# Kernel optimization log

Measured on AMD Instinct MI355X. Metric: run time of the kernel, lower is better.

The kernel has to match this reference:

```python
import jax, jax.numpy as jnp
import numpy as np

NEG_SLOPE = 0.1  # LReLu_neg_slope
WEIGHT_INIT_STD = 1.0
N_GEN, N_LOAD, N_END = 25000, 25000, 25000
N_NODES = 100000
N_EDGES = 1600000
H = 128
N_HIDDEN_LAYERS = 3  # N_GCN_layers - 1


def _lin_w(key, n_in, n_out):
    # torch init: normal(std = weight_init_std / in_channels); stored as (in, out) for jax
    return jax.random.normal(key, (n_in, n_out), dtype=jnp.float32) * (WEIGHT_INIT_STD / n_in)


def setup_inputs() -> dict:
    key = jax.random.key(0)
    ks = jax.random.split(key, 24)
    inp = {
        "x_gen": jax.random.normal(ks[0], (N_GEN, 3), dtype=jnp.float32),
        "x_load": jax.random.normal(ks[1], (N_LOAD, 3), dtype=jnp.float32),
        "x_or": jax.random.normal(ks[2], (N_END, 6), dtype=jnp.float32),
        "x_ex": jax.random.normal(ks[3], (N_END, 6), dtype=jnp.float32),
        "edge_index": jax.random.randint(ks[4], (2, N_EDGES), 0, N_NODES, dtype=jnp.int64)
        if jax.config.jax_enable_x64 else jax.random.randint(ks[4], (2, N_EDGES), 0, N_NODES, dtype=jnp.int32),
        "object_ptv": jnp.arange(N_NODES, dtype=jnp.int32),
    }
    # per-type embedding MLPs (2 Linear layers each)
    inp["Wg1"], inp["bg1"] = _lin_w(ks[5], 3, H), jnp.zeros((H,), jnp.float32)
    inp["Wg2"], inp["bg2"] = _lin_w(ks[6], H, H), jnp.zeros((H,), jnp.float32)
    inp["Wld1"], inp["bld1"] = _lin_w(ks[7], 3, H), jnp.zeros((H,), jnp.float32)
    inp["Wld2"], inp["bld2"] = _lin_w(ks[8], H, H), jnp.zeros((H,), jnp.float32)
    inp["Wor1"], inp["bor1"] = _lin_w(ks[9], 6, H), jnp.zeros((H,), jnp.float32)
    inp["Wor2"], inp["bor2"] = _lin_w(ks[10], H, H), jnp.zeros((H,), jnp.float32)
    inp["Wex1"], inp["bex1"] = _lin_w(ks[11], 6, H), jnp.zeros((H,), jnp.float32)
    inp["Wex2"], inp["bex2"] = _lin_w(ks[12], H, H), jnp.zeros((H,), jnp.float32)
    # hidden SAGEConv layers (stacked): lin_l (neighbor, with bias) + lin_r (root, no bias)
    inp["Wl_h"] = jnp.stack([_lin_w(ks[13 + i], H, H) for i in range(N_HIDDEN_LAYERS)])
    inp["bl_h"] = jnp.zeros((N_HIDDEN_LAYERS, H), jnp.float32)
    inp["Wr_h"] = jnp.stack([_lin_w(ks[16 + i], H, H) for i in range(N_HIDDEN_LAYERS)])
    # output SAGEConv layer -> 1 unit
    inp["Wl_o"], inp["bl_o"] = _lin_w(ks[19], H, 1), jnp.zeros((1,), jnp.float32)
    inp["Wr_o"] = _lin_w(ks[20], H, 1)
    return inp


def _lrelu(x):
    return jax.nn.leaky_relu(x, NEG_SLOPE)


def _embed(x, W1, b1, W2, b2):
    return _lrelu(_lrelu(x @ W1 + b1) @ W2 + b2)


def reference(x_gen, x_load, x_or, x_ex, edge_index, object_ptv,
              Wg1, bg1, Wg2, bg2, Wld1, bld1, Wld2, bld2,
              Wor1, bor1, Wor2, bor2, Wex1, bex1, Wex2, bex2,
              Wl_h, bl_h, Wr_h, Wl_o, bl_o, Wr_o):
    x = jnp.concatenate([
        _embed(x_gen, Wg1, bg1, Wg2, bg2),
        _embed(x_load, Wld1, bld1, Wld2, bld2),
        _embed(x_or, Wor1, bor1, Wor2, bor2),
        _embed(x_ex, Wex1, bex1, Wex2, bex2),
    ], axis=0)
    x = x[object_ptv]                      # [N, H] in topology-vector order
    src, dst = edge_index[0], edge_index[1]
    n = x.shape[0]
    deg = jax.ops.segment_sum(jnp.ones_like(src, dtype=x.dtype), dst, num_segments=n)
    inv_deg = (1.0 / jnp.maximum(deg, 1.0))[:, None]

    def sage(h, Wl, bl, Wr):
        # SAGEConv(aggr='mean', root_weight=True): lin_l(mean_j h_j) + bias + lin_r(h_i)
        agg = jax.ops.segment_sum(h[src], dst, num_segments=n) * inv_deg
        return agg @ Wl + bl + h @ Wr

    for i in range(Wl_h.shape[0]):
        x = _lrelu(sage(x, Wl_h[i], bl_h[i], Wr_h[i]))
    return jax.nn.sigmoid(sage(x, Wl_o, bl_o, Wr_o))  # [N, 1]
```

## Files before the change

### kernel.cpp

```cpp
#include <hip/hip_runtime.h>
#include <hip/hip_bf16.h>
#include <math.h>

#define HD 128
#define NPB 512
#define CAP 16384
#define SCHUNK 4096
#define ALCSR 768

typedef __attribute__((ext_vector_type(8))) short  bf16x8;
typedef __attribute__((ext_vector_type(4))) float  f32x4;

__device__ __forceinline__ float lrelu(float v) { return v > 0.0f ? v : 0.1f * v; }

__device__ __forceinline__ unsigned short f2bf(float f) {
  union { float f; unsigned u; } c; c.f = f;
  unsigned u = c.u + 0x7fffu + ((c.u >> 16) & 1u);
  return (unsigned short)(u >> 16);
}
__device__ __forceinline__ float bf2f(unsigned short u) {
  return __uint_as_float((unsigned)u << 16);
}

__global__ __launch_bounds__(256)
void embed1_kernel(const float* __restrict__ xg, const float* __restrict__ xl,
                   const float* __restrict__ xo, const float* __restrict__ xe,
                   const float* __restrict__ Wg, const float* __restrict__ bg,
                   const float* __restrict__ Wl, const float* __restrict__ bl,
                   const float* __restrict__ Wo, const float* __restrict__ bo,
                   const float* __restrict__ We, const float* __restrict__ be,
                   unsigned short* __restrict__ h1, int4 padCum, int4 realCnt) {
  int p = blockIdx.x * 2 + (threadIdx.x >> 7);
  if (p >= padCum.w) return;
  int j = threadIdx.x & 127;
  int typ = (p < padCum.x) ? 0 : (p < padCum.y) ? 1 : (p < padCum.z) ? 2 : 3;
  int padStart = (typ == 0) ? 0 : (typ == 1) ? padCum.x : (typ == 2) ? padCum.y : padCum.z;
  int cnt = (typ == 0) ? realCnt.x : (typ == 1) ? realCnt.y : (typ == 2) ? realCnt.z : realCnt.w;
  int loc = p - padStart;
  if (loc >= cnt) return;
  const float *x, *W, *bb; int IN;
  if (typ == 0)      { x = xg; W = Wg; bb = bg; IN = 3; }
  else if (typ == 1) { x = xl; W = Wl; bb = bl; IN = 3; }
  else if (typ == 2) { x = xo; W = Wo; bb = bo; IN = 6; }
  else               { x = xe; W = We; bb = be; IN = 6; }
  float acc = bb[j];
  for (int k = 0; k < IN; k++) acc += x[(size_t)loc * IN + k] * W[k * HD + j];
  h1[(size_t)p * HD + j] = f2bf(lrelu(acc));
}

__global__ __launch_bounds__(256)
void wprep_all_kernel(const float* __restrict__ Wg2, const float* __restrict__ Wld2,
                      const float* __restrict__ Wor2, const float* __restrict__ Wex2,
                      const float* __restrict__ Wl_h, const float* __restrict__ Wr_h,
                      unsigned short* __restrict__ Wp,
                      const int* __restrict__ ptv, int* __restrict__ inv,
                      int* __restrict__ gcnt, int n) {
  int tid = blockIdx.x * 256 + threadIdx.x;
  if (tid < 256) gcnt[tid] = 0;
  if (tid < n) inv[ptv[tid]] = tid;
  int m = tid >> 14;
  int i = tid & 16383;
  const float* src; unsigned short* dst;
  switch (m) {
    case 0: src = Wg2;  dst = Wp;             break;
    case 1: src = Wld2; dst = Wp + 16384;     break;
    case 2: src = Wor2; dst = Wp + 2 * 16384; break;
    case 3: src = Wex2; dst = Wp + 3 * 16384; break;
    default: {
      int mm = m - 4; int l = mm >> 1; int isR = mm & 1;
      src = (isR ? Wr_h : Wl_h) + (size_t)l * 16384;
      dst = Wp + 4 * 16384 + (size_t)l * 32768 + (isR ? 16384 : 0);
    }
  }
  int k = i >> 7, j = i & 127;
  int ks = k >> 5, g = (k >> 3) & 3, b = k & 7;
  dst[((ks * 128 + j) * 4 + g) * 8 + b] = f2bf(src[i]);
}

__global__ __launch_bounds__(256)
void mfma_embed2_kernel(const unsigned short* __restrict__ h1,
                        const unsigned short* __restrict__ Wp,
                        const float* __restrict__ b_g, const float* __restrict__ b_ld,
                        const float* __restrict__ b_or, const float* __restrict__ b_ex,
                        const int* __restrict__ inv, unsigned short* __restrict__ out,
                        int4 padCum, int4 realStart, int4 realCnt) {
  const int t = threadIdx.x, w = t >> 6, l = t & 63;
  const int lr = l & 15, lg = l >> 4;
  const int prow0 = blockIdx.x * 64 + w * 16;
  int typ = (prow0 < padCum.x) ? 0 : (prow0 < padCum.y) ? 1 : (prow0 < padCum.z) ? 2 : 3;
  int padStart = (typ == 0) ? 0 : (typ == 1) ? padCum.x : (typ == 2) ? padCum.y : padCum.z;
  int rStart = (typ == 0) ? realStart.x : (typ == 1) ? realStart.y : (typ == 2) ? realStart.z : realStart.w;
  int cnt = (typ == 0) ? realCnt.x : (typ == 1) ? realCnt.y : (typ == 2) ? realCnt.z : realCnt.w;
  const float* bias = (typ == 0) ? b_g : (typ == 1) ? b_ld : (typ == 2) ? b_or : b_ex;

  int raLoc = prow0 + lr - padStart; if (raLoc >= cnt) raLoc = cnt - 1;
  const unsigned short* abase = h1 + (size_t)(padStart + raLoc) * HD + 8 * lg;
  const unsigned short* wbase = Wp + (size_t)typ * 16384 + lr * 32 + lg * 8;

  f32x4 acc[8];
  #pragma unroll
  for (int cb = 0; cb < 8; cb++) {
    float bv = bias[cb * 16 + lr];
    acc[cb] = (f32x4){bv, bv, bv, bv};
  }
  #pragma unroll
  for (int ks = 0; ks < 4; ks++) {
    bf16x8 af = *(const bf16x8*)(abase + ks * 32);
    #pragma unroll
    for (int cb = 0; cb < 8; cb++) {
      bf16x8 bfv = *(const bf16x8*)(wbase + (size_t)(ks * 128 + cb * 16) * 32);
      acc[cb] = __builtin_amdgcn_mfma_f32_16x16x32_bf16(af, bfv, acc[cb], 0, 0, 0);
    }
  }
  int tgt[4];
  #pragma unroll
  for (int r = 0; r < 4; r++) {
    int locRow = prow0 + lg * 4 + r - padStart;
    tgt[r] = (locRow < cnt) ? inv[rStart + locRow] : -1;
  }
  #pragma unroll
  for (int cb = 0; cb < 8; cb++) {
    #pragma unroll
    for (int r = 0; r < 4; r++) {
      if (tgt[r] >= 0)
        out[(size_t)tgt[r] * HD + cb * 16 + lr] = f2bf(lrelu(acc[cb][r]));
    }
  }
}

__global__ __launch_bounds__(256)
void bucket_scatter_kernel(const int* __restrict__ esrc, const int* __restrict__ edst,
                           int* __restrict__ gcnt, int* __restrict__ ebuf, int nE) {
  __shared__ int cnt[256];
  __shared__ int cur[256];
  const int t = threadIdx.x;
  const int c0 = blockIdx.x * SCHUNK;
  int s_arr[16], d_arr[16];
  cnt[t] = 0;
  __syncthreads();
  #pragma unroll
  for (int k = 0; k < 16; k++) {
    int idx = c0 + k * 256 + t;
    if (idx < nE) {
      s_arr[k] = esrc[idx];
      int d = edst[idx];
      d_arr[k] = d;
      atomicAdd(&cnt[d >> 9], 1);
    } else d_arr[k] = -1;
  }
  __syncthreads();
  if (cnt[t] > 0) cur[t] = atomicAdd(&gcnt[t], cnt[t]);
  __syncthreads();
  #pragma unroll
  for (int k = 0; k < 16; k++) {
    if (d_arr[k] >= 0) {
      int b = d_arr[k] >> 9;
      int p = atomicAdd(&cur[b], 1);
      ebuf[(size_t)b * CAP + p] = (s_arr[k] << 9) | (d_arr[k] & 511);
    }
  }
}

__device__ __forceinline__ int wave_incl_scan(int v) {
  int lane = threadIdx.x & 63;
  #pragma unroll
  for (int d = 1; d < 64; d <<= 1) {
    int tv = __shfl_up(v, d, 64);
    if (lane >= d) v += tv;
  }
  return v;
}

__global__ __launch_bounds__(256)
void bucket_build_kernel(const int* __restrict__ ebuf, const int* __restrict__ gcnt,
                         int* __restrict__ csr, int* __restrict__ offs,
                         int* __restrict__ deg, float* __restrict__ inv_deg, int n) {
  __shared__ int hist[512];
  __shared__ int offl[512];
  __shared__ int wsum[4];
  const int b = blockIdx.x, t = threadIdx.x;
  const int cnt = gcnt[b];
  const size_t ebase = (size_t)b * CAP;
  hist[t] = 0; hist[t + 256] = 0;
  __syncthreads();
  for (int i = t; i < cnt; i += 256) {
    int e = ebuf[ebase + i];
    atomicAdd(&hist[e & 511], 1);
  }
  __syncthreads();
  int a0 = hist[2 * t], a1 = hist[2 * t + 1];
  int s = a0 + a1;
  int incl = wave_incl_scan(s);
  int wid = t >> 6;
  if ((t & 63) == 63) wsum[wid] = incl;
  __syncthreads();
  int wbase = 0;
  for (int w_ = 0; w_ < wid; w_++) wbase += wsum[w_];
  int excl = wbase + incl - s;
  offl[2 * t] = excl;
  offl[2 * t + 1] = excl + a0;
  __syncthreads();
  const int d0 = b << 9;
  for (int i = t; i < 512; i += 256) {
    int g = d0 + i;
    if (g < n) {
      offs[g] = b * CAP + offl[i];
      int dg = hist[i];
      deg[g] = dg;
      inv_deg[g] = 1.0f / fmaxf((float)dg, 1.0f);
    }
  }
  __syncthreads();
  for (int i = t; i < cnt; i += 256) {
    int e = ebuf[ebase + i];
    int p = atomicAdd(&offl[e & 511], 1);
    csr[ebase + p] = ((unsigned)e) >> 9;
  }
}

template<bool EMIT_Z>
__global__ __launch_bounds__(256)
void sage_fused_kernel(const unsigned short* __restrict__ x, const int* __restrict__ csr,
                       const int* __restrict__ offs, const int* __restrict__ deg,
                       const float* __restrict__ inv_deg,
                       const unsigned short* __restrict__ Wp, const float* __restrict__ bias,
                       unsigned short* __restrict__ out,
                       const float* __restrict__ wl, const float* __restrict__ wr,
                       float* __restrict__ zl, float* __restrict__ zr, int n) {
  __shared__ int lcsr[ALCSR];
  __shared__ __align__(16) unsigned short lagg[16][136];
  __shared__ float zpart[2][4][16];
  const int t = threadIdx.x;
  const int node0 = blockIdx.x * 16;
  int last = node0 + 15; if (last >= n) last = n - 1;
  const int s_begin = offs[node0];
  const int total = offs[last] + deg[last] - s_begin;
  const bool useLds = (total <= ALCSR);
  if (useLds) {
    for (int k = t; k < total; k += 256) lcsr[k] = csr[s_begin + k];
  }
  __syncthreads();

  const int w = t >> 6, l = t & 63;
  {
    const int g = l >> 4, j = l & 15;
    const int node = node0 + w * 4 + g;
    if (node < n) {
      const unsigned short* xj = x + 8 * j;
      const int lb = offs[node] - s_begin;
      const int d = deg[node];
      float2 a0[4] = {{0.f,0.f},{0.f,0.f},{0.f,0.f},{0.f,0.f}};
      float2 a1[4] = {{0.f,0.f},{0.f,0.f},{0.f,0.f},{0.f,0.f}};
      auto acc4 = [](float2* A, uint4 v) {
        A[0].x += __uint_as_float(v.x << 16); A[0].y += __uint_as_float(v.x & 0xffff0000u);
        A[1].x += __uint_as_float(v.y << 16); A[1].y += __uint_as_float(v.y & 0xffff0000u);
        A[2].x += __uint_as_float(v.z << 16); A[2].y += __uint_as_float(v.z & 0xffff0000u);
        A[3].x += __uint_as_float(v.w << 16); A[3].y += __uint_as_float(v.w & 0xffff0000u);
      };
      int i = 0;
      if (useLds) {
        for (; i + 3 < d; i += 4) {
          int e0 = lcsr[lb + i], e1 = lcsr[lb + i + 1];
          int e2 = lcsr[lb + i + 2], e3 = lcsr[lb + i + 3];
          uint4 v0 = *(const uint4*)(xj + (size_t)e0 * HD);
          uint4 v1 = *(const uint4*)(xj + (size_t)e1 * HD);
          uint4 v2 = *(const uint4*)(xj + (size_t)e2 * HD);
          uint4 v3 = *(const uint4*)(xj + (size_t)e3 * HD);
          acc4(a0, v0); acc4(a1, v1); acc4(a0, v2); acc4(a1, v3);
        }
        if (i + 1 < d) {
          int e0 = lcsr[lb + i], e1 = lcsr[lb + i + 1];
          uint4 v0 = *(const uint4*)(xj + (size_t)e0 * HD);
          uint4 v1 = *(const uint4*)(xj + (size_t)e1 * HD);
          acc4(a0, v0); acc4(a1, v1);
          i += 2;
        }
        if (i < d) {
          int e0 = lcsr[lb + i];
          acc4(a0, *(const uint4*)(xj + (size_t)e0 * HD));
        }
      } else {
        const int* gcsr = csr + s_begin + lb;
        for (; i + 3 < d; i += 4) {
          int e0 = gcsr[i], e1 = gcsr[i + 1], e2 = gcsr[i + 2], e3 = gcsr[i + 3];
          uint4 v0 = *(const uint4*)(xj + (size_t)e0 * HD);
          uint4 v1 = *(const uint4*)(xj + (size_t)e1 * HD);
          uint4 v2 = *(const uint4*)(xj + (size_t)e2 * HD);
          uint4 v3 = *(const uint4*)(xj + (size_t)e3 * HD);
          acc4(a0, v0); acc4(a1, v1); acc4(a0, v2); acc4(a1, v3);
        }
        if (i + 1 < d) {
          int e0 = gcsr[i], e1 = gcsr[i + 1];
          uint4 v0 = *(const uint4*)(xj + (size_t)e0 * HD);
          uint4 v1 = *(const uint4*)(xj + (size_t)e1 * HD);
          acc4(a0, v0); acc4(a1, v1);
          i += 2;
        }
        if (i < d) {
          int e0 = gcsr[i];
          acc4(a0, *(const uint4*)(xj + (size_t)e0 * HD));
        }
      }
      const float id = inv_deg[node];
      uint4 o;
      unsigned* op = (unsigned*)&o;
      #pragma unroll
      for (int k = 0; k < 4; k++) {
        float lo = (a0[k].x + a1[k].x) * id;
        float hi = (a0[k].y + a1[k].y) * id;
        op[k] = (unsigned)f2bf(lo) | ((unsigned)f2bf(hi) << 16);
      }
      *(uint4*)&lagg[w * 4 + g][j * 8] = o;
    } else {
      *(uint4*)&lagg[w * 4 + g][j * 8] = make_uint4(0, 0, 0, 0);
    }
  }
  __syncthreads();

  const int lr = l & 15, lg = l >> 4;
  int ra = node0 + lr; if (ra >= n) ra = n - 1;
  const unsigned short* wbase = Wp + (size_t)lr * 32 + (size_t)lg * 8;
  const unsigned short* rbase = x + (size_t)ra * HD + 8 * lg;

  f32x4 acc[2];
  #pragma unroll
  for (int c = 0; c < 2; c++) {
    float bv = bias[(2 * w + c) * 16 + lr];
    acc[c] = (f32x4){bv, bv, bv, bv};
  }
  #pragma unroll
  for (int ks = 0; ks < 4; ks++) {
    bf16x8 af = *(const bf16x8*)&lagg[lr][lg * 8 + ks * 32];
    #pragma unroll
    for (int c = 0; c < 2; c++) {
      int cb = 2 * w + c;
      bf16x8 bfv = *(const bf16x8*)(wbase + (size_t)(ks * 128 + cb * 16) * 32);
      acc[c] = __builtin_amdgcn_mfma_f32_16x16x32_bf16(af, bfv, acc[c], 0, 0, 0);
    }
  }
  #pragma unroll
  for (int ks = 0; ks < 4; ks++) {
    bf16x8 af = *(const bf16x8*)(rbase + ks * 32);
    #pragma unroll
    for (int c = 0; c < 2; c++) {
      int cb = 2 * w + c;
      bf16x8 bfv = *(const bf16x8*)(wbase + (size_t)((4 + ks) * 128 + cb * 16) * 32);
      acc[c] = __builtin_amdgcn_mfma_f32_16x16x32_bf16(af, bfv, acc[c], 0, 0, 0);
    }
  }

  if constexpr (!EMIT_Z) {
    #pragma unroll
    for (int c = 0; c < 2; c++) {
      int cb = 2 * w + c;
      #pragma unroll
      for (int r = 0; r < 4; r++) {
        int node = node0 + lg * 4 + r;
        if (node < n)
          out[(size_t)node * HD + cb * 16 + lr] = f2bf(lrelu(acc[c][r]));
      }
    }
  } else {
    float vl[4] = {0.f, 0.f, 0.f, 0.f}, vr[4] = {0.f, 0.f, 0.f, 0.f};
    #pragma unroll
    for (int c = 0; c < 2; c++) {
      int cb = 2 * w + c;
      float wlv = wl[cb * 16 + lr];
      float wrv = wr[cb * 16 + lr];
      #pragma unroll
      for (int r = 0; r < 4; r++) {
        float x3 = lrelu(acc[c][r]);
        vl[r] += x3 * wlv;
        vr[r] += x3 * wrv;
      }
    }
    #pragma unroll
    for (int r = 0; r < 4; r++) {
      #pragma unroll
      for (int d = 1; d < 16; d <<= 1) {
        vl[r] += __shfl_xor(vl[r], d, 64);
        vr[r] += __shfl_xor(vr[r], d, 64);
      }
    }
    if (lr == 0) {
      #pragma unroll
      for (int r = 0; r < 4; r++) {
        zpart[0][w][lg * 4 + r] = vl[r];
        zpart[1][w][lg * 4 + r] = vr[r];
      }
    }
    __syncthreads();
    if (t < 16) {
      int node = node0 + t;
      if (node < n) {
        zl[node] = zpart[0][0][t] + zpart[0][1][t] + zpart[0][2][t] + zpart[0][3][t];
        zr[node] = zpart[1][0][t] + zpart[1][1][t] + zpart[1][2][t] + zpart[1][3][t];
      }
    }
  }
}

__global__ __launch_bounds__(256)
void zfinal_kernel(const float* __restrict__ zl, const float* __restrict__ zr,
                   const int* __restrict__ csr, const int* __restrict__ offs,
                   const int* __restrict__ deg, const float* __restrict__ inv_deg,
                   const float* __restrict__ bl, float* __restrict__ out, int n) {
  int i = blockIdx.x * 256 + threadIdx.x;
  if (i >= n) return;
  int s0 = offs[i], d = deg[i];
  float a = 0.f;
  #pragma unroll 4
  for (int e = 0; e < d; e++) a += zl[csr[s0 + e]];
  float s = a * inv_deg[i] + bl[0] + zr[i];
  out[i] = 1.0f / (1.0f + expf(-s));
}

extern "C" void kernel_launch(void* const* d_in, const int* in_sizes, int n_in,
                              void* d_out, int out_size, void* d_ws, size_t ws_size,
                              hipStream_t stream) {
  const float* x_gen  = (const float*)d_in[0];
  const float* x_load = (const float*)d_in[1];
  const float* x_or   = (const float*)d_in[2];
  const float* x_ex   = (const float*)d_in[3];
  const int*   edge   = (const int*)d_in[4];
  const int*   ptv    = (const int*)d_in[5];
  const float* Wg1  = (const float*)d_in[6],  *bg1  = (const float*)d_in[7];
  const float* Wg2  = (const float*)d_in[8],  *bg2  = (const float*)d_in[9];
  const float* Wld1 = (const float*)d_in[10], *bld1 = (const float*)d_in[11];
  const float* Wld2 = (const float*)d_in[12], *bld2 = (const float*)d_in[13];
  const float* Wor1 = (const float*)d_in[14], *bor1 = (const float*)d_in[15];
  const float* Wor2 = (const float*)d_in[16], *bor2 = (const float*)d_in[17];
  const float* Wex1 = (const float*)d_in[18], *bex1 = (const float*)d_in[19];
  const float* Wex2 = (const float*)d_in[20], *bex2 = (const float*)d_in[21];
  const float* Wl_h = (const float*)d_in[22], *bl_h = (const float*)d_in[23];
  const float* Wr_h = (const float*)d_in[24];
  const float* Wl_o = (const float*)d_in[25], *bl_o = (const float*)d_in[26];
  const float* Wr_o = (const float*)d_in[27];

  const int n_gen  = in_sizes[0] / 3;
  const int n_load = in_sizes[1] / 3;
  const int n_or   = in_sizes[2] / 6;
  const int n_ex   = in_sizes[3] / 6;
  const int nE     = in_sizes[4] / 2;
  const int N      = in_sizes[5];
  const int* esrc = edge;
  const int* edst = edge + nE;

  const int np0 = ((n_gen  + 63) / 64) * 64;
  const int np1 = ((n_load + 63) / 64) * 64;
  const int np2 = ((n_or   + 63) / 64) * 64;
  const int np3 = ((n_ex   + 63) / 64) * 64;
  const int NP  = np0 + np1 + np2 + np3;
  const int4 padCum    = make_int4(np0, np0 + np1, np0 + np1 + np2, NP);
  const int4 realStart = make_int4(0, n_gen, n_gen + n_load, n_gen + n_load + n_or);
  const int4 realCnt   = make_int4(n_gen, n_load, n_or, n_ex);

  const int NB = (N + NPB - 1) / NPB;

  size_t NPel = (size_t)NP * HD;
  size_t nel  = (size_t)N * HD;
  unsigned short* b0 = (unsigned short*)d_ws;
  unsigned short* b1 = b0 + NPel;
  unsigned short* b3 = b1 + nel;
  int*  gcnt = (int*)(b3 + nel);
  int*  ebuf = gcnt + 256;
  int*  csr  = ebuf + (size_t)NB * CAP;
  int*  offs = csr + (size_t)NB * CAP;
  int*  deg  = offs + N;
  float* inv_deg = (float*)(deg + N);
  float* zl = inv_deg + N;
  float* zr = zl + N;
  int*  invp = (int*)(zr + N);
  uintptr_t wp_addr = ((uintptr_t)(invp + N) + 15) & ~(uintptr_t)15;
  unsigned short* Wp = (unsigned short*)wp_addr;

  wprep_all_kernel<<<640, 256, 0, stream>>>(Wg2, Wld2, Wor2, Wex2, Wl_h, Wr_h, Wp,
                                            ptv, invp, gcnt, N);

  embed1_kernel<<<NP / 2, 256, 0, stream>>>(x_gen, x_load, x_or, x_ex,
                                            Wg1, bg1, Wld1, bld1, Wor1, bor1, Wex1, bex1,
                                            b0, padCum, realCnt);
  mfma_embed2_kernel<<<NP / 64, 256, 0, stream>>>(b0, Wp, bg2, bld2, bor2, bex2,
                                                  invp, b1, padCum, realStart, realCnt);

  bucket_scatter_kernel<<<(nE + SCHUNK - 1) / SCHUNK, 256, 0, stream>>>(esrc, edst, gcnt, ebuf, nE);
  bucket_build_kernel<<<NB, 256, 0, stream>>>(ebuf, gcnt, csr, offs, deg, inv_deg, N);

  const int fGrid = (N + 15) / 16;
  const unsigned short* WpC = Wp + 4 * 16384;
  unsigned short* xcur = b1;
  unsigned short* xnext = b3;
  for (int l = 0; l < 2; l++) {
    sage_fused_kernel<false><<<fGrid, 256, 0, stream>>>(
        xcur, csr, offs, deg, inv_deg, WpC + (size_t)l * 32768,
        bl_h + (size_t)l * HD, xnext, nullptr, nullptr, nullptr, nullptr, N);
    unsigned short* tmp = xcur; xcur = xnext; xnext = tmp;
  }
  sage_fused_kernel<true><<<fGrid, 256, 0, stream>>>(
      xcur, csr, offs, deg, inv_deg, WpC + 2 * 32768,
      bl_h + 2 * HD, nullptr, Wl_o, Wr_o, zl, zr, N);

  zfinal_kernel<<<(N + 255) / 256, 256, 0, stream>>>(zl, zr, csr, offs, deg, inv_deg,
                                                     bl_o, (float*)d_out, N);
}
```

Before: 347.0 us.

## Gather neighbor features in FP8 E5M2 to halve aggregation bandwidth

Keeps a second copy of node features in FP8 E5M2, produced by a new conversion kernel after the embedding and written alongside the bf16 output of each hidden SAGE layer. The neighbor-mean gather then reads 8 bytes per lane instead of 16, aiming to cut memory traffic in the bandwidth-bound aggregation. The cost is an extra conversion pass, extra byte stores, and a large loss of precision in the aggregated features that may break accuracy tolerance. The root term still uses the bf16 copy.

```diff
diff --git a/kernel.cpp b/kernel.cpp
--- a/kernel.cpp
+++ b/kernel.cpp
@@ -1,5 +1,6 @@
 #include <hip/hip_runtime.h>
 #include <hip/hip_bf16.h>
+#include <hip/hip_fp16.h>
 #include <math.h>
 
 #define HD 128
@@ -20,6 +21,14 @@
 }
 __device__ __forceinline__ float bf2f(unsigned short u) {
   return __uint_as_float((unsigned)u << 16);
+}
+__device__ __forceinline__ unsigned char f2e5m2(float f) {
+  unsigned short h = __half_as_ushort(__float2half(f));
+  h = (unsigned short)(h + 0x7f + ((h >> 8) & 1));
+  return (unsigned char)(h >> 8);
+}
+__device__ __forceinline__ float e5m2hi2f(unsigned u) {
+  return __half2float(__ushort_as_half((unsigned short)u));
 }
 
 __global__ __launch_bounds__(256)
@@ -129,6 +138,25 @@
 }
 
 __global__ __launch_bounds__(256)
+void bf2f8_kernel(const unsigned short* __restrict__ in, unsigned char* __restrict__ out, int n8) {
+  int idx = blockIdx.x * 256 + threadIdx.x;
+  if (idx >= n8) return;
+  uint4 v = *(const uint4*)(in + (size_t)idx * 8);
+  unsigned char b0 = f2e5m2(__uint_as_float(v.x << 16));
+  unsigned char b1 = f2e5m2(__uint_as_float(v.x & 0xffff0000u));
+  unsigned char b2 = f2e5m2(__uint_as_float(v.y << 16));
+  unsigned char b3 = f2e5m2(__uint_as_float(v.y & 0xffff0000u));
+  unsigned char b4 = f2e5m2(__uint_as_float(v.z << 16));
+  unsigned char b5 = f2e5m2(__uint_as_float(v.z & 0xffff0000u));
+  unsigned char b6 = f2e5m2(__uint_as_float(v.w << 16));
+  unsigned char b7 = f2e5m2(__uint_as_float(v.w & 0xffff0000u));
+  uint2 o;
+  o.x = (unsigned)b0 | ((unsigned)b1 << 8) | ((unsigned)b2 << 16) | ((unsigned)b3 << 24);
+  o.y = (unsigned)b4 | ((unsigned)b5 << 8) | ((unsigned)b6 << 16) | ((unsigned)b7 << 24);
+  *(uint2*)(out + (size_t)idx * 8) = o;
+}
+
+__global__ __launch_bounds__(256)
 void bucket_scatter_kernel(const int* __restrict__ esrc, const int* __restrict__ edst,
                            int* __restrict__ gcnt, int* __restrict__ ebuf, int nE) {
   __shared__ int cnt[256];
@@ -220,11 +248,12 @@
 
 template<bool EMIT_Z>
 __global__ __launch_bounds__(256)
-void sage_fused_kernel(const unsigned short* __restrict__ x, const int* __restrict__ csr,
+void sage_fused_kernel(const unsigned short* __restrict__ x, const unsigned char* __restrict__ xf8,
+                       const int* __restrict__ csr,
                        const int* __restrict__ offs, const int* __restrict__ deg,
                        const float* __restrict__ inv_deg,
                        const unsigned short* __restrict__ Wp, const float* __restrict__ bias,
-                       unsigned short* __restrict__ out,
+                       unsigned short* __restrict__ out, unsigned char* __restrict__ outf8,
                        const float* __restrict__ wl, const float* __restrict__ wr,
                        float* __restrict__ zl, float* __restrict__ zr, int n) {
   __shared__ int lcsr[ALCSR];
@@ -246,59 +275,63 @@
     const int g = l >> 4, j = l & 15;
     const int node = node0 + w * 4 + g;
     if (node < n) {
-      const unsigned short* xj = x + 8 * j;
+      const unsigned char* xj = xf8 + 8 * j;
       const int lb = offs[node] - s_begin;
       const int d = deg[node];
       float2 a0[4] = {{0.f,0.f},{0.f,0.f},{0.f,0.f},{0.f,0.f}};
       float2 a1[4] = {{0.f,0.f},{0.f,0.f},{0.f,0.f},{0.f,0.f}};
-      auto acc4 = [](float2* A, uint4 v) {
-        A[0].x += __uint_as_float(v.x << 16); A[0].y += __uint_as_float(v.x & 0xffff0000u);
-        A[1].x += __uint_as_float(v.y << 16); A[1].y += __uint_as_float(v.y & 0xffff0000u);
-        A[2].x += __uint_as_float(v.z << 16); A[2].y += __uint_as_float(v.z & 0xffff0000u);
-        A[3].x += __uint_as_float(v.w << 16); A[3].y += __uint_as_float(v.w & 0xffff0000u);
+      auto acc8 = [](float2* A, uint2 v) {
+        A[0].x += e5m2hi2f((v.x << 8) & 0xff00u);
+        A[0].y += e5m2hi2f(v.x & 0xff00u);
+        A[1].x += e5m2hi2f((v.x >> 8) & 0xff00u);
+        A[1].y += e5m2hi2f((v.x >> 16) & 0xff00u);
+        A[2].x += e5m2hi2f((v.y << 8) & 0xff00u);
+        A[2].y += e5m2hi2f(v.y & 0xff00u);
+        A[3].x += e5m2hi2f((v.y >> 8) & 0xff00u);
+        A[3].y += e5m2hi2f((v.y >> 16) & 0xff00u);
       };
       int i = 0;
       if (useLds) {
         for (; i + 3 < d; i += 4) {
           int e0 = lcsr[lb + i], e1 = lcsr[lb + i + 1];
           int e2 = lcsr[lb + i + 2], e3 = lcsr[lb + i + 3];
-          uint4 v0 = *(const uint4*)(xj + (size_t)e0 * HD);
-          uint4 v1 = *(const uint4*)(xj + (size_t)e1 * HD);
-          uint4 v2 = *(const uint4*)(xj + (size_t)e2 * HD);
-          uint4 v3 = *(const uint4*)(xj + (size_t)e3 * HD);
-          acc4(a0, v0); acc4(a1, v1); acc4(a0, v2); acc4(a1, v3);
+          uint2 v0 = *(const uint2*)(xj + (size_t)e0 * HD);
+          uint2 v1 = *(const uint2*)(xj + (size_t)e1 * HD);
+          uint2 v2 = *(const uint2*)(xj + (size_t)e2 * HD);
+          uint2 v3 = *(const uint2*)(xj + (size_t)e3 * HD);
+          acc8(a0, v0); acc8(a1, v1); acc8(a0, v2); acc8(a1, v3);
         }
         if (i + 1 < d) {
           int e0 = lcsr[lb + i], e1 = lcsr[lb + i + 1];
-          uint4 v0 = *(const uint4*)(xj + (size_t)e0 * HD);
-          uint4 v1 = *(const uint4*)(xj + (size_t)e1 * HD);
-          acc4(a0, v0); acc4(a1, v1);
+          uint2 v0 = *(const uint2*)(xj + (size_t)e0 * HD);
+          uint2 v1 = *(const uint2*)(xj + (size_t)e1 * HD);
+          acc8(a0, v0); acc8(a1, v1);
           i += 2;
         }
         if (i < d) {
           int e0 = lcsr[lb + i];
-          acc4(a0, *(const uint4*)(xj + (size_t)e0 * HD));
+          acc8(a0, *(const uint2*)(xj + (size_t)e0 * HD));
         }
       } else {
         const int* gcsr = csr + s_begin + lb;
         for (; i + 3 < d; i += 4) {
           int e0 = gcsr[i], e1 = gcsr[i + 1], e2 = gcsr[i + 2], e3 = gcsr[i + 3];
-          uint4 v0 = *(const uint4*)(xj + (size_t)e0 * HD);
-          uint4 v1 = *(const uint4*)(xj + (size_t)e1 * HD);
-          uint4 v2 = *(const uint4*)(xj + (size_t)e2 * HD);
-          uint4 v3 = *(const uint4*)(xj + (size_t)e3 * HD);
-          acc4(a0, v0); acc4(a1, v1); acc4(a0, v2); acc4(a1, v3);
+          uint2 v0 = *(const uint2*)(xj + (size_t)e0 * HD);
+          uint2 v1 = *(const uint2*)(xj + (size_t)e1 * HD);
+          uint2 v2 = *(const uint2*)(xj + (size_t)e2 * HD);
+          uint2 v3 = *(const uint2*)(xj + (size_t)e3 * HD);
+          acc8(a0, v0); acc8(a1, v1); acc8(a0, v2); acc8(a1, v3);
         }
         if (i + 1 < d) {
           int e0 = gcsr[i], e1 = gcsr[i + 1];
-          uint4 v0 = *(const uint4*)(xj + (size_t)e0 * HD);
-          uint4 v1 = *(const uint4*)(xj + (size_t)e1 * HD);
-          acc4(a0, v0); acc4(a1, v1);
+          uint2 v0 = *(const uint2*)(xj + (size_t)e0 * HD);
+          uint2 v1 = *(const uint2*)(xj + (size_t)e1 * HD);
+          acc8(a0, v0); acc8(a1, v1);
           i += 2;
         }
         if (i < d) {
           int e0 = gcsr[i];
-          acc4(a0, *(const uint4*)(xj + (size_t)e0 * HD));
+          acc8(a0, *(const uint2*)(xj + (size_t)e0 * HD));
         }
       }
       const float id = inv_deg[node];
@@ -356,8 +389,11 @@
       #pragma unroll
       for (int r = 0; r < 4; r++) {
         int node = node0 + lg * 4 + r;
-        if (node < n)
-          out[(size_t)node * HD + cb * 16 + lr] = f2bf(lrelu(acc[c][r]));
+        if (node < n) {
+          float val = lrelu(acc[c][r]);
+          out[(size_t)node * HD + cb * 16 + lr] = f2bf(val);
+          outf8[(size_t)node * HD + cb * 16 + lr] = f2e5m2(val);
+        }
       }
     }
   } else {
@@ -473,6 +509,9 @@
   int*  invp = (int*)(zr + N);
   uintptr_t wp_addr = ((uintptr_t)(invp + N) + 15) & ~(uintptr_t)15;
   unsigned short* Wp = (unsigned short*)wp_addr;
+  uintptr_t f8_addr = ((uintptr_t)(Wp + 4 * 16384 + 3 * 32768) + 15) & ~(uintptr_t)15;
+  unsigned char* f8a = (unsigned char*)f8_addr;
+  unsigned char* f8b = f8a + nel;
 
   wprep_all_kernel<<<640, 256, 0, stream>>>(Wg2, Wld2, Wor2, Wex2, Wl_h, Wr_h, Wp,
                                             ptv, invp, gcnt, N);
@@ -482,23 +521,25 @@
                                             b0, padCum, realCnt);
   mfma_embed2_kernel<<<NP / 64, 256, 0, stream>>>(b0, Wp, bg2, bld2, bor2, bex2,
                                                   invp, b1, padCum, realStart, realCnt);
+  bf2f8_kernel<<<(N * 16 + 255) / 256, 256, 0, stream>>>(b1, f8a, N * 16);
 
   bucket_scatter_kernel<<<(nE + SCHUNK - 1) / SCHUNK, 256, 0, stream>>>(esrc, edst, gcnt, ebuf, nE);
   bucket_build_kernel<<<NB, 256, 0, stream>>>(ebuf, gcnt, csr, offs, deg, inv_deg, N);
 
   const int fGrid = (N + 15) / 16;
   const unsigned short* WpC = Wp + 4 * 16384;
-  unsigned short* xcur = b1;
-  unsigned short* xnext = b3;
+  unsigned short* xbf = b1;  unsigned char* xf8 = f8a;
+  unsigned short* nbf = b3;  unsigned char* nf8 = f8b;
   for (int l = 0; l < 2; l++) {
     sage_fused_kernel<false><<<fGrid, 256, 0, stream>>>(
-        xcur, csr, offs, deg, inv_deg, WpC + (size_t)l * 32768,
-        bl_h + (size_t)l * HD, xnext, nullptr, nullptr, nullptr, nullptr, N);
-    unsigned short* tmp = xcur; xcur = xnext; xnext = tmp;
+        xbf, xf8, csr, offs, deg, inv_deg, WpC + (size_t)l * 32768,
+        bl_h + (size_t)l * HD, nbf, nf8, nullptr, nullptr, nullptr, nullptr, N);
+    unsigned short* tb = xbf; xbf = nbf; nbf = tb;
+    unsigned char*  tf = xf8; xf8 = nf8; nf8 = tf;
   }
   sage_fused_kernel<true><<<fGrid, 256, 0, stream>>>(
-      xcur, csr, offs, deg, inv_deg, WpC + 2 * 32768,
-      bl_h + 2 * HD, nullptr, Wl_o, Wr_o, zl, zr, N);
+      xbf, xf8, csr, offs, deg, inv_deg, WpC + 2 * 32768,
+      bl_h + 2 * HD, nullptr, nullptr, Wl_o, Wr_o, zl, zr, N);
 
   zfinal_kernel<<<(N + 255) / 256, 256, 0, stream>>>(zl, zr, csr, offs, deg, inv_deg,
                                                      bl_o, (float*)d_out, N);
```

Result: faster. 331.1 us (-4.6%).
